# Optimization experiments

Measured on AMD Instinct MI355X. Metric: run time of the kernel, lower is better.

## Reference

```python
import jax, jax.numpy as jnp
import numpy as np

START_TAG = 0
END_TAG = 63
NEG_INF = -10000.0


def setup_inputs() -> dict:
    key = jax.random.key(0)
    k1, k2, k3 = jax.random.split(key, 3)
    S, D, L = 32768, 1024, 64  # seq_len, feature_dim, num_labels
    feats = jax.random.normal(k1, (S, D), jnp.float32)
    W = jax.random.normal(k2, (L, D), jnp.float32) * 0.02  # nn.Linear weight [out,in]
    b = jnp.zeros((L,), jnp.float32)
    transitions = jax.random.normal(k3, (L, L), jnp.float32)
    transitions = transitions.at[START_TAG, :].set(NEG_INF).at[:, END_TAG].set(NEG_INF)
    return {"feats": feats, "W": W, "b": b, "transitions": transitions}


def reference(feats, W, b, transitions):
    # emissions: [S, L]
    emissions = feats @ W.T + b

    # Viterbi forward pass.  scores[j] after step t = best path score ending in label j.
    init_scores = transitions[:, START_TAG] + emissions[0]

    def step(scores, emit):
        # swt[j, i] = scores[i] + T[j, i]  (transition i -> j)
        swt = scores[None, :] + transitions  # [L, L]
        new_scores = emit + jnp.max(swt, axis=-1)
        back_ptr = jnp.argmax(swt, axis=-1)
        return new_scores, back_ptr

    final_scores, back_ptrs = jax.lax.scan(step, init_scores, emissions[1:])
    final_scores = final_scores + transitions[END_TAG]

    viterbi_score = jnp.max(final_scores)
    last_tag = jnp.argmax(final_scores)

    # Backtrack: tag[t-1] = back_ptrs[t-1][tag[t]] (back_ptrs[k] is for time k+1).
    def back(tag, bp):
        return bp[tag], tag

    first_tag, rest_tags = jax.lax.scan(back, last_tag, back_ptrs, reverse=True)
    tag_seq = jnp.concatenate([first_tag[None], rest_tags])  # [S]
    return viterbi_score, tag_seq
```

## Files before the change

### kernel.cpp

```cpp
#include <hip/hip_runtime.h>

#define S_LEN 32768
#define D_DIM 1024
#define L_LAB 64
#define LC 32
#define NCH (S_LEN / LC)
#define H_WARM 32
#define CHUNK 128
#define NCHUNK (S_LEN / CHUNK)

#define EM_OFF   0
#define SC_OFF   (S_LEN * 64 * 4)
#define BP_OFF   (SC_OFF + S_LEN * 64 * 4)
#define MAPS_OFF (BP_OFF + S_LEN * 64)
#define BND_OFF  (MAPS_OFF + NCHUNK * 64)
#define WIN_OFF  (BND_OFF + 256)
#define WBF_OFF  (WIN_OFF + NCH * 4)

typedef __attribute__((ext_vector_type(8))) short short8;
typedef __attribute__((ext_vector_type(4))) float floatx4;

__device__ inline unsigned short f32_bf16_rne(float f) {
    unsigned v = __float_as_uint(f);
    v += 0x7FFFu + ((v >> 16) & 1u);
    return (unsigned short)(v >> 16);
}

__global__ __launch_bounds__(256) void wconv_kernel(
        const float* __restrict__ W, unsigned short* __restrict__ Wbf) {
    int i = blockIdx.x * 256 + threadIdx.x;
    Wbf[i] = f32_bf16_rne(W[i]);
}

__global__ __launch_bounds__(256) __attribute__((amdgpu_waves_per_eu(2, 2)))
void emis_kernel(
        const float* __restrict__ feats, const unsigned short* __restrict__ Wbf,
        const float* __restrict__ bvec, float* __restrict__ em) {
    __shared__ __align__(16) unsigned short As[64 * 72];
    __shared__ __align__(16) unsigned short Bs[64 * 72];

    const int tid = threadIdx.x;
    const int lan = tid & 15;
    const int q   = (tid >> 4) & 3;
    const int w   = tid >> 6;
    const int row0 = blockIdx.x * 64;

    floatx4 acc[4];
#pragma unroll
    for (int nt = 0; nt < 4; ++nt) acc[nt] = (floatx4){0.f, 0.f, 0.f, 0.f};

    for (int kb = 0; kb < D_DIM; kb += 64) {
        __syncthreads();
#pragma unroll
        for (int i = 0; i < 4; ++i) {
            int gi = tid + i * 256;
            int m = gi >> 4, g = gi & 15;
            float4 v = *(const float4*)&feats[(size_t)(row0 + m) * D_DIM + kb + g * 4];
            unsigned h0 = f32_bf16_rne(v.x) | ((unsigned)f32_bf16_rne(v.y) << 16);
            unsigned h1 = f32_bf16_rne(v.z) | ((unsigned)f32_bf16_rne(v.w) << 16);
            *(uint2*)&As[m * 72 + g * 4] = (uint2){h0, h1};
        }
#pragma unroll
        for (int i = 0; i < 2; ++i) {
            int gi = tid + i * 256;
            int m = gi >> 3, g = gi & 7;
            *(uint4*)&Bs[m * 72 + g * 8] =
                *(const uint4*)&Wbf[(size_t)m * D_DIM + kb + g * 8];
        }
        __syncthreads();

#pragma unroll
        for (int cc = 0; cc < 2; ++cc) {
            int koff = cc * 32 + q * 8;
            int m_loc = w * 16 + lan;
            short8 av = *(const short8*)&As[m_loc * 72 + koff];
#pragma unroll
            for (int nt = 0; nt < 4; ++nt) {
                int label = nt * 16 + lan;
                short8 bv = *(const short8*)&Bs[label * 72 + koff];
                acc[nt] = __builtin_amdgcn_mfma_f32_16x16x32_bf16(av, bv, acc[nt], 0, 0, 0);
            }
        }
    }

#pragma unroll
    for (int nt = 0; nt < 4; ++nt) {
        int label = nt * 16 + lan;
        float bias = bvec[label];
#pragma unroll
        for (int r = 0; r < 4; ++r) {
            int row = row0 + w * 16 + q * 4 + r;
            em[(size_t)row * 64 + label] = acc[nt][r] + bias;
        }
    }
}

__global__ __launch_bounds__(64) __attribute__((amdgpu_waves_per_eu(1, 1)))
void fwd_chunks(
        const float* __restrict__ em, const float* __restrict__ T,
        float* __restrict__ sc_hist, float* __restrict__ win) {
    const int j = threadIdx.x;
    const int c = blockIdx.x;
    const int a = c * LC;
    const int bend = a + LC;

    float Trow[64];
#pragma unroll
    for (int i = 0; i < 16; ++i)
        ((float4*)Trow)[i] = ((const float4*)(T + j * 64))[i];

    int t0 = a - 1 - H_WARM;
    if (t0 < 0) t0 = 0;

    float sc;
    if (t0 == 0) {
        sc = Trow[0] + em[j];
        if (c == 0) sc_hist[j] = sc;
    } else {
        sc = em[(size_t)t0 * 64 + j];
    }

    auto step = [&](float e) {
        float v[16];
#pragma unroll
        for (int k = 0; k < 16; ++k) {
            float a0 = __int_as_float(__builtin_amdgcn_readlane(__float_as_int(sc), k)) + Trow[k];
            float a1 = __int_as_float(__builtin_amdgcn_readlane(__float_as_int(sc), k + 16)) + Trow[k + 16];
            float a2 = __int_as_float(__builtin_amdgcn_readlane(__float_as_int(sc), k + 32)) + Trow[k + 32];
            float a3 = __int_as_float(__builtin_amdgcn_readlane(__float_as_int(sc), k + 48)) + Trow[k + 48];
            v[k] = fmaxf(fmaxf(fmaxf(a0, a1), a2), a3);
        }
        float r0 = fmaxf(fmaxf(v[0], v[1]), v[2]);
        float r1 = fmaxf(fmaxf(v[3], v[4]), v[5]);
        float r2 = fmaxf(fmaxf(v[6], v[7]), v[8]);
        float r3 = fmaxf(fmaxf(v[9], v[10]), v[11]);
        float r4 = fmaxf(fmaxf(v[12], v[13]), v[14]);
        float s0 = fmaxf(fmaxf(r0, r1), r2);
        float s1 = fmaxf(fmaxf(r3, r4), v[15]);
        sc = e + fmaxf(s0, s1);
    };

    int t = t0 + 1;
    if (t < a) {
        float p0 = em[(size_t)(t + 0) * 64 + j];
        float p1 = em[(size_t)(t + 1) * 64 + j];
        float p2 = em[(size_t)(t + 2) * 64 + j];
        float p3 = em[(size_t)(t + 3) * 64 + j];
        for (; t + 3 < a; t += 4) {
            float n0 = em[(size_t)(t + 4) * 64 + j];
            float n1 = em[(size_t)(t + 5) * 64 + j];
            float n2 = em[(size_t)(t + 6) * 64 + j];
            float n3 = em[(size_t)(t + 7) * 64 + j];
            step(p0); step(p1); step(p2); step(p3);
            p0 = n0; p1 = n1; p2 = n2; p3 = n3;
        }
        for (; t < a; ++t) { step(p0); p0 = p1; p1 = p2; p2 = p3; }
    }
    if (c > 0 && j == 0) win[c] = sc;

    t = (a > 0) ? a : 1;
    {
        float p0 = em[(size_t)(t + 0) * 64 + j];
        float p1 = em[(size_t)(t + 1) * 64 + j];
        float p2 = em[(size_t)(t + 2) * 64 + j];
        float p3 = em[(size_t)(t + 3) * 64 + j];
        for (; t + 3 < bend; t += 4) {
            int t4 = t + 4 > S_LEN - 1 ? S_LEN - 1 : t + 4;
            int t5 = t + 5 > S_LEN - 1 ? S_LEN - 1 : t + 5;
            int t6 = t + 6 > S_LEN - 1 ? S_LEN - 1 : t + 6;
            int t7 = t + 7 > S_LEN - 1 ? S_LEN - 1 : t + 7;
            float n0 = em[(size_t)t4 * 64 + j];
            float n1 = em[(size_t)t5 * 64 + j];
            float n2 = em[(size_t)t6 * 64 + j];
            float n3 = em[(size_t)t7 * 64 + j];
            step(p0); sc_hist[(size_t)(t + 0) * 64 + j] = sc;
            step(p1); sc_hist[(size_t)(t + 1) * 64 + j] = sc;
            step(p2); sc_hist[(size_t)(t + 2) * 64 + j] = sc;
            step(p3); sc_hist[(size_t)(t + 3) * 64 + j] = sc;
            p0 = n0; p1 = n1; p2 = n2; p3 = n3;
        }
        for (; t < bend; ++t) {
            step(p0); sc_hist[(size_t)t * 64 + j] = sc;
            p0 = p1; p1 = p2; p2 = p3;
        }
    }
}

__global__ __launch_bounds__(256) __attribute__((amdgpu_waves_per_eu(2, 2)))
void bp_maps_kernel(
        const float* __restrict__ sc_hist, const float* __restrict__ T,
        unsigned char* __restrict__ bp, unsigned char* __restrict__ maps) {
    __shared__ unsigned char lb[CHUNK * 64];
    const int tid = threadIdx.x;
    const int j = tid & 63;
    const int w = tid >> 6;
    const int c = blockIdx.x;
    const int base = c * CHUNK;

    float Trow[64];
#pragma unroll
    for (int i = 0; i < 16; ++i)
        ((float4*)Trow)[i] = ((const float4*)(T + j * 64))[i];

    for (int k = 0; k < CHUNK / 4; ++k) {
        int tt = w * (CHUNK / 4) + k;
        int t = base + tt;
        int bi = 0;
        if (t >= 1) {
            const float* prev = sc_hist + (size_t)(t - 1) * 64;
            float best = 0.f;
#pragma unroll
            for (int i = 0; i < 64; ++i) {
                float v = prev[i] + Trow[i];
                if (i == 0) best = v;
                else if (v > best) { best = v; bi = i; }
            }
        }
        lb[tt * 64 + j] = (unsigned char)bi;
    }
    __syncthreads();

    uint4* dst = (uint4*)(bp + (size_t)base * 64);
    const uint4* src = (const uint4*)lb;
#pragma unroll
    for (int i = 0; i < 2; ++i) dst[tid + i * 256] = src[tid + i * 256];

    if (tid < 64) {
        int x = tid;
        for (int tt = CHUNK - 1; tt >= 0; --tt) {
            if (base + tt >= 1) x = lb[tt * 64 + x];
        }
        maps[c * 64 + tid] = (unsigned char)x;
    }
}

__global__ __launch_bounds__(256) void finish_kernel(
        const float* __restrict__ sc_hist, const float* __restrict__ T,
        const float* __restrict__ win, const unsigned char* __restrict__ maps,
        float* __restrict__ out, unsigned char* __restrict__ bnd) {
    __shared__ unsigned char lm[NCHUNK * 64];
    __shared__ int lt;
    int tid = threadIdx.x;
    const uint4* src = (const uint4*)maps;
    uint4* dst = (uint4*)lm;
#pragma unroll
    for (int i = 0; i < (NCHUNK * 64 / 16) / 256; ++i) dst[tid + i * 256] = src[tid + i * 256];

    if (tid < 64) {
        int j = tid;
        float part = 0.f;
        for (int c = 1 + j; c < NCH; c += 64) {
            float end_prev = sc_hist[((size_t)c * LC - 1) * 64 + 0];
            part += end_prev - win[c];
        }
#pragma unroll
        for (int off = 32; off; off >>= 1) part += __shfl_xor(part, off, 64);

        float f = sc_hist[(size_t)(S_LEN - 1) * 64 + j] + T[63 * 64 + j];
        float best = 0.f; int bt = 0;
#pragma unroll
        for (int k = 0; k < 64; ++k) {
            float fv = __int_as_float(__builtin_amdgcn_readlane(__float_as_int(f), k));
            if (k == 0) best = fv;
            else if (fv > best) { best = fv; bt = k; }
        }
        if (j == 0) { out[0] = best + part; lt = bt; }
    }
    __syncthreads();
    if (tid == 0) {
        int x = lt;
        bnd[NCHUNK - 1] = (unsigned char)x;
        for (int c = NCHUNK - 1; c >= 1; --c) {
            x = lm[c * 64 + x];
            bnd[c - 1] = (unsigned char)x;
        }
    }
}

__global__ __launch_bounds__(64) void bt_fill(
        const unsigned char* __restrict__ bp, const unsigned char* __restrict__ bnd,
        float* __restrict__ out) {
    __shared__ unsigned char lb[CHUNK * 64];
    int c = blockIdx.x, l = threadIdx.x;
    const uint4* src = (const uint4*)(bp + (size_t)c * CHUNK * 64);
    uint4* dst = (uint4*)lb;
#pragma unroll
    for (int i = 0; i < (CHUNK * 64 / 16) / 64; ++i) dst[l + i * 64] = src[l + i * 64];
    __syncthreads();
    if (l == 0) {
        int t0 = c * CHUNK;
        int x = bnd[c];
        out[1 + t0 + CHUNK - 1] = (float)x;
        for (int tt = CHUNK - 1; tt >= 0; --tt) {
            int t = t0 + tt;
            if (t >= 1) {
                x = lb[tt * 64 + x];
                out[1 + t - 1] = (float)x;
            }
        }
    }
}

extern "C" void kernel_launch(void* const* d_in, const int* in_sizes, int n_in,
                              void* d_out, int out_size, void* d_ws, size_t ws_size,
                              hipStream_t stream) {
    const float* feats = (const float*)d_in[0];
    const float* W     = (const float*)d_in[1];
    const float* b     = (const float*)d_in[2];
    const float* T     = (const float*)d_in[3];
    float* out = (float*)d_out;

    char* ws = (char*)d_ws;
    float*          em       = (float*)(ws + EM_OFF);
    float*          sc_hist  = (float*)(ws + SC_OFF);
    unsigned char*  bp       = (unsigned char*)(ws + BP_OFF);
    unsigned char*  maps     = (unsigned char*)(ws + MAPS_OFF);
    unsigned char*  bnd      = (unsigned char*)(ws + BND_OFF);
    float*          win      = (float*)(ws + WIN_OFF);
    unsigned short* Wbf      = (unsigned short*)(ws + WBF_OFF);

    wconv_kernel<<<(L_LAB * D_DIM) / 256, 256, 0, stream>>>(W, Wbf);
    emis_kernel<<<S_LEN / 64, 256, 0, stream>>>(feats, Wbf, b, em);
    fwd_chunks<<<NCH, 64, 0, stream>>>(em, T, sc_hist, win);
    bp_maps_kernel<<<NCHUNK, 256, 0, stream>>>(sc_hist, T, bp, maps);
    finish_kernel<<<1, 256, 0, stream>>>(sc_hist, T, win, maps, out, bnd);
    bt_fill<<<NCHUNK, 64, 0, stream>>>(bp, bnd, out);
}
```

Before: 306.5 us.

## Fuse backpointer and chunk-map computation into forward pass, drop score history

The forward chunk kernel now computes argmax backpointers inline, packing the index into the low mantissa bits of biased scores. It writes byte backpointers and per-chunk composed maps via ds_bpermute, so the float score-history buffer and the separate bp_maps kernel are no longer needed. The finish kernel composes maps hierarchically with 1024 threads instead of a serial single-thread chain, and bt_fill uses lane-parallel readlane chains per 32-step chunk. The warmup length is halved. The extra work is integer max operations in the sequential step. The 32768 bias trick truncates low mantissa bits, so near-ties may be broken differently from the reference argmax.

```diff
diff --git a/kernel.cpp b/kernel.cpp
--- a/kernel.cpp
+++ b/kernel.cpp
@@ -5,17 +5,18 @@
 #define L_LAB 64
 #define LC 32
 #define NCH (S_LEN / LC)
-#define H_WARM 32
-#define CHUNK 128
-#define NCHUNK (S_LEN / CHUNK)
+#define H_WARM 16
+#define NSUP 32
+#define SUPC 32
 
 #define EM_OFF   0
-#define SC_OFF   (S_LEN * 64 * 4)
-#define BP_OFF   (SC_OFF + S_LEN * 64 * 4)
+#define BP_OFF   (S_LEN * 64 * 4)
 #define MAPS_OFF (BP_OFF + S_LEN * 64)
-#define BND_OFF  (MAPS_OFF + NCHUNK * 64)
-#define WIN_OFF  (BND_OFF + 256)
-#define WBF_OFF  (WIN_OFF + NCH * 4)
+#define BND_OFF  (MAPS_OFF + NCH * 64)
+#define WIN_OFF  (BND_OFF + 1024)
+#define END_OFF  (WIN_OFF + NCH * 4)
+#define FIN_OFF  (END_OFF + NCH * 4)
+#define WBF_OFF  (FIN_OFF + 256)
 
 typedef __attribute__((ext_vector_type(8))) short short8;
 typedef __attribute__((ext_vector_type(4))) float floatx4;
@@ -25,6 +26,7 @@
     v += 0x7FFFu + ((v >> 16) & 1u);
     return (unsigned short)(v >> 16);
 }
+__device__ inline int imax(int a, int b) { return a > b ? a : b; }
 
 __global__ __launch_bounds__(256) void wconv_kernel(
         const float* __restrict__ W, unsigned short* __restrict__ Wbf) {
@@ -98,7 +100,9 @@
 __global__ __launch_bounds__(64) __attribute__((amdgpu_waves_per_eu(1, 1)))
 void fwd_chunks(
         const float* __restrict__ em, const float* __restrict__ T,
-        float* __restrict__ sc_hist, float* __restrict__ win) {
+        unsigned char* __restrict__ bp, unsigned char* __restrict__ maps,
+        float* __restrict__ win, float* __restrict__ endsc,
+        float* __restrict__ finrow) {
     const int j = threadIdx.x;
     const int c = blockIdx.x;
     const int a = c * LC;
@@ -108,14 +112,15 @@
 #pragma unroll
     for (int i = 0; i < 16; ++i)
         ((float4*)Trow)[i] = ((const float4*)(T + j * 64))[i];
+#pragma unroll
+    for (int i = 0; i < 64; ++i) Trow[i] += 32768.0f;
 
     int t0 = a - 1 - H_WARM;
     if (t0 < 0) t0 = 0;
 
     float sc;
     if (t0 == 0) {
-        sc = Trow[0] + em[j];
-        if (c == 0) sc_hist[j] = sc;
+        sc = Trow[0] + (em[j] - 32768.0f);
     } else {
         sc = em[(size_t)t0 * 64 + j];
     }
@@ -140,17 +145,45 @@
         sc = e + fmaxf(s0, s1);
     };
 
+    int bi = 0;
+    auto stepx = [&](float e) {
+        float v[16];
+        int m0 = 0, m1 = 0, m2 = 0, m3 = 0;
+#pragma unroll
+        for (int k = 0; k < 16; ++k) {
+            float a0 = __int_as_float(__builtin_amdgcn_readlane(__float_as_int(sc), k)) + Trow[k];
+            float a1 = __int_as_float(__builtin_amdgcn_readlane(__float_as_int(sc), k + 16)) + Trow[k + 16];
+            float a2 = __int_as_float(__builtin_amdgcn_readlane(__float_as_int(sc), k + 32)) + Trow[k + 32];
+            float a3 = __int_as_float(__builtin_amdgcn_readlane(__float_as_int(sc), k + 48)) + Trow[k + 48];
+            m0 = imax(m0, (__float_as_int(a0) & ~63) | (63 - k));
+            m1 = imax(m1, (__float_as_int(a1) & ~63) | (63 - (k + 16)));
+            m2 = imax(m2, (__float_as_int(a2) & ~63) | (63 - (k + 32)));
+            m3 = imax(m3, (__float_as_int(a3) & ~63) | (63 - (k + 48)));
+            v[k] = fmaxf(fmaxf(fmaxf(a0, a1), a2), a3);
+        }
+        float r0 = fmaxf(fmaxf(v[0], v[1]), v[2]);
+        float r1 = fmaxf(fmaxf(v[3], v[4]), v[5]);
+        float r2 = fmaxf(fmaxf(v[6], v[7]), v[8]);
+        float r3 = fmaxf(fmaxf(v[9], v[10]), v[11]);
+        float r4 = fmaxf(fmaxf(v[12], v[13]), v[14]);
+        float s0 = fmaxf(fmaxf(r0, r1), r2);
+        float s1 = fmaxf(fmaxf(r3, r4), v[15]);
+        sc = e + fmaxf(s0, s1);
+        int mm = imax(imax(m0, m1), imax(m2, m3));
+        bi = 63 - (mm & 63);
+    };
+
     int t = t0 + 1;
     if (t < a) {
-        float p0 = em[(size_t)(t + 0) * 64 + j];
-        float p1 = em[(size_t)(t + 1) * 64 + j];
-        float p2 = em[(size_t)(t + 2) * 64 + j];
-        float p3 = em[(size_t)(t + 3) * 64 + j];
+        float p0 = em[(size_t)(t + 0) * 64 + j] - 32768.0f;
+        float p1 = em[(size_t)(t + 1) * 64 + j] - 32768.0f;
+        float p2 = em[(size_t)(t + 2) * 64 + j] - 32768.0f;
+        float p3 = em[(size_t)(t + 3) * 64 + j] - 32768.0f;
         for (; t + 3 < a; t += 4) {
-            float n0 = em[(size_t)(t + 4) * 64 + j];
-            float n1 = em[(size_t)(t + 5) * 64 + j];
-            float n2 = em[(size_t)(t + 6) * 64 + j];
-            float n3 = em[(size_t)(t + 7) * 64 + j];
+            float n0 = em[(size_t)(t + 4) * 64 + j] - 32768.0f;
+            float n1 = em[(size_t)(t + 5) * 64 + j] - 32768.0f;
+            float n2 = em[(size_t)(t + 6) * 64 + j] - 32768.0f;
+            float n3 = em[(size_t)(t + 7) * 64 + j] - 32768.0f;
             step(p0); step(p1); step(p2); step(p3);
             p0 = n0; p1 = n1; p2 = n2; p3 = n3;
         }
@@ -158,147 +191,142 @@
     }
     if (c > 0 && j == 0) win[c] = sc;
 
+    int fmap = j;
     t = (a > 0) ? a : 1;
     {
-        float p0 = em[(size_t)(t + 0) * 64 + j];
-        float p1 = em[(size_t)(t + 1) * 64 + j];
-        float p2 = em[(size_t)(t + 2) * 64 + j];
-        float p3 = em[(size_t)(t + 3) * 64 + j];
+        float p0 = em[(size_t)(t + 0) * 64 + j] - 32768.0f;
+        float p1 = em[(size_t)(t + 1) * 64 + j] - 32768.0f;
+        float p2 = em[(size_t)(t + 2) * 64 + j] - 32768.0f;
+        float p3 = em[(size_t)(t + 3) * 64 + j] - 32768.0f;
         for (; t + 3 < bend; t += 4) {
             int t4 = t + 4 > S_LEN - 1 ? S_LEN - 1 : t + 4;
             int t5 = t + 5 > S_LEN - 1 ? S_LEN - 1 : t + 5;
             int t6 = t + 6 > S_LEN - 1 ? S_LEN - 1 : t + 6;
             int t7 = t + 7 > S_LEN - 1 ? S_LEN - 1 : t + 7;
-            float n0 = em[(size_t)t4 * 64 + j];
-            float n1 = em[(size_t)t5 * 64 + j];
-            float n2 = em[(size_t)t6 * 64 + j];
-            float n3 = em[(size_t)t7 * 64 + j];
-            step(p0); sc_hist[(size_t)(t + 0) * 64 + j] = sc;
-            step(p1); sc_hist[(size_t)(t + 1) * 64 + j] = sc;
-            step(p2); sc_hist[(size_t)(t + 2) * 64 + j] = sc;
-            step(p3); sc_hist[(size_t)(t + 3) * 64 + j] = sc;
+            float n0 = em[(size_t)t4 * 64 + j] - 32768.0f;
+            float n1 = em[(size_t)t5 * 64 + j] - 32768.0f;
+            float n2 = em[(size_t)t6 * 64 + j] - 32768.0f;
+            float n3 = em[(size_t)t7 * 64 + j] - 32768.0f;
+            stepx(p0); bp[(size_t)(t + 0) * 64 + j] = (unsigned char)bi;
+            fmap = __builtin_amdgcn_ds_bpermute(bi << 2, fmap);
+            stepx(p1); bp[(size_t)(t + 1) * 64 + j] = (unsigned char)bi;
+            fmap = __builtin_amdgcn_ds_bpermute(bi << 2, fmap);
+            stepx(p2); bp[(size_t)(t + 2) * 64 + j] = (unsigned char)bi;
+            fmap = __builtin_amdgcn_ds_bpermute(bi << 2, fmap);
+            stepx(p3); bp[(size_t)(t + 3) * 64 + j] = (unsigned char)bi;
+            fmap = __builtin_amdgcn_ds_bpermute(bi << 2, fmap);
             p0 = n0; p1 = n1; p2 = n2; p3 = n3;
         }
         for (; t < bend; ++t) {
-            step(p0); sc_hist[(size_t)t * 64 + j] = sc;
+            stepx(p0); bp[(size_t)t * 64 + j] = (unsigned char)bi;
+            fmap = __builtin_amdgcn_ds_bpermute(bi << 2, fmap);
             p0 = p1; p1 = p2; p2 = p3;
         }
     }
-}
-
-__global__ __launch_bounds__(256) __attribute__((amdgpu_waves_per_eu(2, 2)))
-void bp_maps_kernel(
-        const float* __restrict__ sc_hist, const float* __restrict__ T,
-        unsigned char* __restrict__ bp, unsigned char* __restrict__ maps) {
-    __shared__ unsigned char lb[CHUNK * 64];
+
+    maps[c * 64 + j] = (unsigned char)fmap;
+    if (j == 0) endsc[c] = sc;
+    if (c == NCH - 1) finrow[j] = sc;
+}
+
+__global__ __launch_bounds__(1024) void finish_kernel(
+        const float* __restrict__ T, const float* __restrict__ win,
+        const float* __restrict__ endsc, const float* __restrict__ finrow,
+        const unsigned char* __restrict__ maps, float* __restrict__ out,
+        unsigned char* __restrict__ bnd) {
+    __shared__ unsigned char sm[NSUP * 64];
+    __shared__ unsigned char sbl[NSUP];
+    __shared__ float psum[16];
     const int tid = threadIdx.x;
-    const int j = tid & 63;
-    const int w = tid >> 6;
-    const int c = blockIdx.x;
-    const int base = c * CHUNK;
-
-    float Trow[64];
-#pragma unroll
-    for (int i = 0; i < 16; ++i)
-        ((float4*)Trow)[i] = ((const float4*)(T + j * 64))[i];
-
-    for (int k = 0; k < CHUNK / 4; ++k) {
-        int tt = w * (CHUNK / 4) + k;
-        int t = base + tt;
-        int bi = 0;
-        if (t >= 1) {
-            const float* prev = sc_hist + (size_t)(t - 1) * 64;
-            float best = 0.f;
-#pragma unroll
-            for (int i = 0; i < 64; ++i) {
-                float v = prev[i] + Trow[i];
-                if (i == 0) best = v;
-                else if (v > best) { best = v; bi = i; }
-            }
-        }
-        lb[tt * 64 + j] = (unsigned char)bi;
+    const int lane = tid & 63;
+    const int wid = tid >> 6;
+
+    float p = 0.f;
+    if (tid >= 1 && tid < NCH) p = endsc[tid - 1] - win[tid];
+#pragma unroll
+    for (int off = 32; off; off >>= 1) p += __shfl_xor(p, off, 64);
+    if (lane == 0) psum[wid] = p;
+
+#pragma unroll
+    for (int r = 0; r < 2; ++r) {
+        int s = wid * 2 + r;
+        int x = lane;
+#pragma unroll 4
+        for (int q = SUPC - 1; q >= 0; --q) {
+            int mq = maps[(s * SUPC + q) * 64 + lane];
+            x = __builtin_amdgcn_ds_bpermute(x << 2, mq);
+        }
+        sm[s * 64 + lane] = (unsigned char)x;
     }
     __syncthreads();
 
-    uint4* dst = (uint4*)(bp + (size_t)base * 64);
-    const uint4* src = (const uint4*)lb;
-#pragma unroll
-    for (int i = 0; i < 2; ++i) dst[tid + i * 256] = src[tid + i * 256];
-
     if (tid < 64) {
-        int x = tid;
-        for (int tt = CHUNK - 1; tt >= 0; --tt) {
-            if (base + tt >= 1) x = lb[tt * 64 + x];
-        }
-        maps[c * 64 + tid] = (unsigned char)x;
-    }
-}
-
-__global__ __launch_bounds__(256) void finish_kernel(
-        const float* __restrict__ sc_hist, const float* __restrict__ T,
-        const float* __restrict__ win, const unsigned char* __restrict__ maps,
-        float* __restrict__ out, unsigned char* __restrict__ bnd) {
-    __shared__ unsigned char lm[NCHUNK * 64];
-    __shared__ int lt;
-    int tid = threadIdx.x;
-    const uint4* src = (const uint4*)maps;
-    uint4* dst = (uint4*)lm;
-#pragma unroll
-    for (int i = 0; i < (NCHUNK * 64 / 16) / 256; ++i) dst[tid + i * 256] = src[tid + i * 256];
-
-    if (tid < 64) {
-        int j = tid;
         float part = 0.f;
-        for (int c = 1 + j; c < NCH; c += 64) {
-            float end_prev = sc_hist[((size_t)c * LC - 1) * 64 + 0];
-            part += end_prev - win[c];
-        }
-#pragma unroll
-        for (int off = 32; off; off >>= 1) part += __shfl_xor(part, off, 64);
-
-        float f = sc_hist[(size_t)(S_LEN - 1) * 64 + j] + T[63 * 64 + j];
-        float best = 0.f; int bt = 0;
+#pragma unroll
+        for (int i = 0; i < 16; ++i) part += psum[i];
+
+        float f = finrow[lane] + T[63 * 64 + lane];
+        float best = 0.f; int bt_ = 0;
 #pragma unroll
         for (int k = 0; k < 64; ++k) {
             float fv = __int_as_float(__builtin_amdgcn_readlane(__float_as_int(f), k));
             if (k == 0) best = fv;
-            else if (fv > best) { best = fv; bt = k; }
-        }
-        if (j == 0) { out[0] = best + part; lt = bt; }
+            else if (fv > best) { best = fv; bt_ = k; }
+        }
+        if (lane == 0) out[0] = best + part;
+
+        int rows[NSUP];
+#pragma unroll
+        for (int s = 0; s < NSUP; ++s) rows[s] = sm[s * 64 + lane];
+        int x = bt_;
+        int sbv = 0;
+        if (lane == NSUP - 1) sbv = x;
+#pragma unroll
+        for (int s = NSUP - 1; s >= 1; --s) {
+            x = __builtin_amdgcn_readlane(rows[s], x);
+            if (lane == s - 1) sbv = x;
+        }
+        if (lane < NSUP) sbl[lane] = (unsigned char)sbv;
     }
     __syncthreads();
-    if (tid == 0) {
-        int x = lt;
-        bnd[NCHUNK - 1] = (unsigned char)x;
-        for (int c = NCHUNK - 1; c >= 1; --c) {
-            x = lm[c * 64 + x];
-            bnd[c - 1] = (unsigned char)x;
-        }
+
+#pragma unroll
+    for (int r = 0; r < 2; ++r) {
+        int s = wid * 2 + r;
+        int rows[SUPC];
+#pragma unroll
+        for (int q = 1; q < SUPC; ++q)
+            rows[q] = maps[(s * SUPC + q) * 64 + lane];
+        int x = __builtin_amdgcn_readfirstlane((int)sbl[s]);
+        int bv = 0;
+        if (lane == SUPC - 1) bv = x;
+#pragma unroll
+        for (int q = SUPC - 1; q >= 1; --q) {
+            x = __builtin_amdgcn_readlane(rows[q], x);
+            if (lane == q - 1) bv = x;
+        }
+        if (lane < SUPC) bnd[s * SUPC + lane] = (unsigned char)bv;
     }
 }
 
 __global__ __launch_bounds__(64) void bt_fill(
         const unsigned char* __restrict__ bp, const unsigned char* __restrict__ bnd,
         float* __restrict__ out) {
-    __shared__ unsigned char lb[CHUNK * 64];
-    int c = blockIdx.x, l = threadIdx.x;
-    const uint4* src = (const uint4*)(bp + (size_t)c * CHUNK * 64);
-    uint4* dst = (uint4*)lb;
-#pragma unroll
-    for (int i = 0; i < (CHUNK * 64 / 16) / 64; ++i) dst[l + i * 64] = src[l + i * 64];
-    __syncthreads();
-    if (l == 0) {
-        int t0 = c * CHUNK;
-        int x = bnd[c];
-        out[1 + t0 + CHUNK - 1] = (float)x;
-        for (int tt = CHUNK - 1; tt >= 0; --tt) {
-            int t = t0 + tt;
-            if (t >= 1) {
-                x = lb[tt * 64 + x];
-                out[1 + t - 1] = (float)x;
-            }
-        }
-    }
+    const int c = blockIdx.x;
+    const int lane = threadIdx.x;
+    int rows[LC];
+#pragma unroll
+    for (int tt = 1; tt < LC; ++tt)
+        rows[tt] = bp[((size_t)c * LC + tt) * 64 + lane];
+    int x = __builtin_amdgcn_readfirstlane((int)bnd[c]);
+    int tv = 0;
+    if (lane == LC - 1) tv = x;
+#pragma unroll
+    for (int tt = LC - 1; tt >= 1; --tt) {
+        x = __builtin_amdgcn_readlane(rows[tt], x);
+        if (lane == tt - 1) tv = x;
+    }
+    if (lane < LC) out[1 + c * LC + lane] = (float)tv;
 }
 
 extern "C" void kernel_launch(void* const* d_in, const int* in_sizes, int n_in,
@@ -311,18 +339,18 @@
     float* out = (float*)d_out;
 
     char* ws = (char*)d_ws;
-    float*          em       = (float*)(ws + EM_OFF);
-    float*          sc_hist  = (float*)(ws + SC_OFF);
-    unsigned char*  bp       = (unsigned char*)(ws + BP_OFF);
-    unsigned char*  maps     = (unsigned char*)(ws + MAPS_OFF);
-    unsigned char*  bnd      = (unsigned char*)(ws + BND_OFF);
-    float*          win      = (float*)(ws + WIN_OFF);
-    unsigned short* Wbf      = (unsigned short*)(ws + WBF_OFF);
+    float*          em     = (float*)(ws + EM_OFF);
+    unsigned char*  bp     = (unsigned char*)(ws + BP_OFF);
+    unsigned char*  maps   = (unsigned char*)(ws + MAPS_OFF);
+    unsigned char*  bnd    = (unsigned char*)(ws + BND_OFF);
+    float*          win    = (float*)(ws + WIN_OFF);
+    float*          endsc  = (float*)(ws + END_OFF);
+    float*          finrow = (float*)(ws + FIN_OFF);
+    unsigned short* Wbf    = (unsigned short*)(ws + WBF_OFF);
 
     wconv_kernel<<<(L_LAB * D_DIM) / 256, 256, 0, stream>>>(W, Wbf);
     emis_kernel<<<S_LEN / 64, 256, 0, stream>>>(feats, Wbf, b, em);
-    fwd_chunks<<<NCH, 64, 0, stream>>>(em, T, sc_hist, win);
-    bp_maps_kernel<<<NCHUNK, 256, 0, stream>>>(sc_hist, T, bp, maps);
-    finish_kernel<<<1, 256, 0, stream>>>(sc_hist, T, win, maps, out, bnd);
-    bt_fill<<<NCHUNK, 64, 0, stream>>>(bp, bnd, out);
-}
+    fwd_chunks<<<NCH, 64, 0, stream>>>(em, T, bp, maps, win, endsc, finrow);
+    finish_kernel<<<1, 1024, 0, stream>>>(T, win, endsc, finrow, maps, out, bnd);
+    bt_fill<<<NCH, 64, 0, stream>>>(bp, bnd, out);
+}
```

After: 254.3 us. -17.0%, faster.
